# Kernel tuning notes

Hardware: AMD Instinct MI355X
Metric: run time of the kernel (lower is better)

## Reference

```python
import jax, jax.numpy as jnp
import numpy as np

N = 50000

def gcn_conv(x, W, b, src, dst, n_nodes):
    # PyG GCNConv: h = x @ W; add self-loops; sym-normalize; scatter-add; + bias
    h = x @ W  # [N, d_out]
    loop = jnp.arange(n_nodes, dtype=src.dtype)
    s = jnp.concatenate([src, loop])
    d = jnp.concatenate([dst, loop])
    deg = jax.ops.segment_sum(jnp.ones_like(d, dtype=h.dtype), d, num_segments=n_nodes)
    dinv = jnp.where(deg > 0, jax.lax.rsqrt(deg), 0.0)
    norm = dinv[s] * dinv[d]  # [E+N]
    msgs = h[s] * norm[:, None]  # gather + scale
    out = jax.ops.segment_sum(msgs, d, num_segments=n_nodes)  # scatter-add
    return out + b

def setup_inputs() -> dict:
    key = jax.random.key(0)
    k1, k2, k3, k4 = jax.random.split(key, 4)
    in_c, hid_c, out_c, E = 512, 256, 64, 800000
    x = jax.random.normal(k1, (N, in_c), dtype=jnp.float32)
    edge_index = jax.random.randint(k2, (2, E), 0, N, dtype=jnp.int64)
    W1 = jax.random.normal(k3, (in_c, hid_c), dtype=jnp.float32) / np.sqrt(in_c)
    b1 = jnp.zeros((hid_c,), dtype=jnp.float32)
    W2 = jax.random.normal(k4, (hid_c, out_c), dtype=jnp.float32) / np.sqrt(hid_c)
    b2 = jnp.zeros((out_c,), dtype=jnp.float32)
    return {"x": x, "edge_index": edge_index, "W1": W1, "b1": b1, "W2": W2, "b2": b2}

def reference(x, edge_index, W1, b1, W2, b2):
    src, dst = edge_index[0], edge_index[1]
    h = gcn_conv(x, W1, b1, src, dst, N)
    h = jax.nn.relu(h)
    h = gcn_conv(h, W2, b2, src, dst, N)
    return jax.nn.log_softmax(h, axis=1)
```

## Files before the change

kernel.cpp:

```cpp
#include <hip/hip_runtime.h>
#include <hip/hip_bf16.h>

#define IN_C 512
#define HID_C 256
#define OUT_C 64

typedef __attribute__((ext_vector_type(8))) short bf16x8;
typedef __attribute__((ext_vector_type(4))) float f32x4;

__device__ __forceinline__ ushort f2bf(float f) {
  __hip_bfloat16 h = __float2bfloat16(f);
  union { __hip_bfloat16 h; ushort u; } v; v.h = h; return v.u;
}
__device__ __forceinline__ void acc2(float& lo, float& hi, uint u) {
  union { uint i; float f; } a, b;
  a.i = u << 16; b.i = u & 0xffff0000u;
  lo += a.f; hi += b.f;
}


__global__ void deg_count(const int* __restrict__ dst, int* __restrict__ counts, int E) {
  int e = blockIdx.x * 256 + threadIdx.x;
  if (e >= E) return;
  atomicAdd(&counts[dst[e]], 1);
}

#define SCAN_TILE 1024

__global__ __launch_bounds__(256) void scan_block_sums(const int* __restrict__ counts,
                                                       int* __restrict__ partial, int n) {
  int base = blockIdx.x * SCAN_TILE + threadIdx.x * 4;
  int s = 0;
  if (base + 3 < n) {
    int4 v = *(const int4*)(counts + base);
    s = v.x + v.y + v.z + v.w;
  } else {
#pragma unroll
    for (int i = 0; i < 4; ++i) if (base + i < n) s += counts[base + i];
  }
#pragma unroll
  for (int off = 1; off < 64; off <<= 1) s += __shfl_xor(s, off);
  __shared__ int ws[4];
  int lane = threadIdx.x & 63, wid = threadIdx.x >> 6;
  if (lane == 0) ws[wid] = s;
  __syncthreads();
  if (threadIdx.x == 0) partial[blockIdx.x] = ws[0] + ws[1] + ws[2] + ws[3];
}

__global__ void scan_partials(int* __restrict__ partial, int nb) {
  int lane = threadIdx.x;
  int carry = 0;
  for (int base = 0; base < nb; base += 64) {
    int i = base + lane;
    int v = (i < nb) ? partial[i] : 0;
    int incl = v;
#pragma unroll
    for (int off = 1; off < 64; off <<= 1) {
      int y = __shfl_up(incl, off);
      if (lane >= off) incl += y;
    }
    if (i < nb) partial[i] = carry + incl - v;
    carry += __shfl(incl, 63);
  }
}

__global__ __launch_bounds__(256) void scan_write(const int* __restrict__ counts,
                                                  const int* __restrict__ partial,
                                                  int* __restrict__ offs,
                                                  int* __restrict__ cur,
                                                  float* __restrict__ dinv,
                                                  int n, int E) {
  int tid = threadIdx.x;
  int base = blockIdx.x * SCAN_TILE + tid * 4;
  int4 c = make_int4(0, 0, 0, 0);
  if (base + 3 < n) {
    c = *(const int4*)(counts + base);
  } else {
    if (base + 0 < n) c.x = counts[base + 0];
    if (base + 1 < n) c.y = counts[base + 1];
    if (base + 2 < n) c.z = counts[base + 2];
  }
  int tsum = c.x + c.y + c.z + c.w;
  int lane = tid & 63, wid = tid >> 6;
  int incl = tsum;
#pragma unroll
  for (int off = 1; off < 64; off <<= 1) {
    int y = __shfl_up(incl, off);
    if (lane >= off) incl += y;
  }
  __shared__ int ws[4];
  if (lane == 63) ws[wid] = incl;
  __syncthreads();
  int wbase = 0;
#pragma unroll
  for (int w = 0; w < 4; ++w) if (w < wid) wbase += ws[w];
  int off0 = partial[blockIdx.x] + wbase + (incl - tsum);
  int4 ov;
  ov.x = off0;
  ov.y = off0 + c.x;
  ov.z = off0 + c.x + c.y;
  ov.w = off0 + c.x + c.y + c.z;
  float4 dv;
  dv.x = rsqrtf((float)(c.x + 1));
  dv.y = rsqrtf((float)(c.y + 1));
  dv.z = rsqrtf((float)(c.z + 1));
  dv.w = rsqrtf((float)(c.w + 1));
  if (base + 3 < n) {
    *(int4*)(offs + base) = ov;
    *(int4*)(cur + base) = ov;
    *(float4*)(dinv + base) = dv;
  } else {
    int o4[4] = {ov.x, ov.y, ov.z, ov.w};
    float d4[4] = {dv.x, dv.y, dv.z, dv.w};
    for (int i = 0; i < 4; ++i)
      if (base + i < n) { offs[base + i] = o4[i]; cur[base + i] = o4[i]; dinv[base + i] = d4[i]; }
  }
  if (blockIdx.x == 0 && tid == 0) offs[n] = E;
}

__global__ void fill_adj(const int* __restrict__ src, const int* __restrict__ dst,
                         int* __restrict__ cur, int* __restrict__ adj, int E) {
  int e = blockIdx.x * 256 + threadIdx.x;
  if (e >= E) return;
  int pos = atomicAdd(&cur[dst[e]], 1);
  adj[pos] = src[e];
}

__global__ void convert_wt(const float* __restrict__ W, ushort* __restrict__ Wt, int K, int Ncol) {
  int idx = blockIdx.x * 256 + threadIdx.x;
  if (idx >= K * Ncol) return;
  int n = idx / K, k = idx % K;
  Wt[idx] = f2bf(W[(size_t)k * Ncol + n]);
}


#define LDP 56

__global__ __launch_bounds__(256) void gemm1(const float* __restrict__ A,
                                             const ushort* __restrict__ Bt,
                                             const float* __restrict__ dinv,
                                             ushort* __restrict__ C, int M) {
  __shared__ __align__(16) short As[128 * LDP];
  __shared__ __align__(16) short Bs[128 * LDP];
  int tid = threadIdx.x;
  int m0 = blockIdx.x * 128;
  int n0 = blockIdx.y * 128;
  int lane = tid & 63, wid = tid >> 6;
  int wm = (wid >> 1) * 64, wn = (wid & 1) * 64;
  f32x4 acc[4][4] = {};
  for (int k0 = 0; k0 < IN_C; k0 += 32) {
    {
      int tr = tid >> 3;
      int tc = (tid & 7) * 4;
#pragma unroll
      for (int i = 0; i < 4; ++i) {
        int row = tr + i * 32;
        int gm = m0 + row;
        float4 v = make_float4(0.f, 0.f, 0.f, 0.f);
        if (gm < M) v = *(const float4*)(A + (size_t)gm * IN_C + k0 + tc);
        uint2 p;
        p.x = (uint)f2bf(v.x) | ((uint)f2bf(v.y) << 16);
        p.y = (uint)f2bf(v.z) | ((uint)f2bf(v.w) << 16);
        *(uint2*)&As[row * LDP + tc] = p;
      }
    }
    {
#pragma unroll
      for (int i = 0; i < 2; ++i) {
        int chunk = tid + i * 256;
        int row = chunk >> 2;
        int c8 = (chunk & 3) * 8;
        uint4 v = *(const uint4*)(Bt + (size_t)(n0 + row) * IN_C + k0 + c8);
        *(uint4*)&Bs[row * LDP + c8] = v;
      }
    }
    __syncthreads();
    bf16x8 a[4], b[4];
    int kf = (lane >> 4) * 8;
    int rl = lane & 15;
#pragma unroll
    for (int i = 0; i < 4; ++i)
      a[i] = *(const bf16x8*)&As[(wm + i * 16 + rl) * LDP + kf];
#pragma unroll
    for (int j = 0; j < 4; ++j)
      b[j] = *(const bf16x8*)&Bs[(wn + j * 16 + rl) * LDP + kf];
#pragma unroll
    for (int i = 0; i < 4; ++i)
#pragma unroll
      for (int j = 0; j < 4; ++j)
        acc[i][j] = __builtin_amdgcn_mfma_f32_16x16x32_bf16(a[i], b[j], acc[i][j], 0, 0, 0);
    __syncthreads();
  }
  int r4 = (lane >> 4) * 4;
  int cl = lane & 15;
#pragma unroll
  for (int i = 0; i < 4; ++i) {
#pragma unroll
    for (int r = 0; r < 4; ++r) {
      int gr = m0 + wm + i * 16 + r4 + r;
      if (gr < M) {
        float dv = dinv[gr];
#pragma unroll
        for (int j = 0; j < 4; ++j) {
          int gc = n0 + wn + j * 16 + cl;
          C[(size_t)gr * HID_C + gc] = f2bf(dv * acc[i][j][r]);
        }
      }
    }
  }
}

__global__ __launch_bounds__(256) void gemm2(const ushort* __restrict__ A,
                                             const ushort* __restrict__ Bt,
                                             const float* __restrict__ dinv,
                                             ushort* __restrict__ C, int M) {
  __shared__ __align__(16) short As[128 * LDP];
  __shared__ __align__(16) short Bs[64 * LDP];
  int tid = threadIdx.x;
  int m0 = blockIdx.x * 128;
  int lane = tid & 63, wid = tid >> 6;
  int wm = wid * 32;
  f32x4 acc[2][4] = {};
  for (int k0 = 0; k0 < HID_C; k0 += 32) {
    {
#pragma unroll
      for (int i = 0; i < 2; ++i) {
        int chunk = tid + i * 256;
        int row = chunk >> 2;
        int c8 = (chunk & 3) * 8;
        int gm = m0 + row;
        uint4 v = make_uint4(0u, 0u, 0u, 0u);
        if (gm < M) v = *(const uint4*)(A + (size_t)gm * HID_C + k0 + c8);
        *(uint4*)&As[row * LDP + c8] = v;
      }
    }
    {
      int chunk = tid;
      int row = chunk >> 2;
      int c8 = (chunk & 3) * 8;
      uint4 v = *(const uint4*)(Bt + (size_t)row * HID_C + k0 + c8);
      *(uint4*)&Bs[row * LDP + c8] = v;
    }
    __syncthreads();
    bf16x8 a[2], b[4];
    int kf = (lane >> 4) * 8;
    int rl = lane & 15;
#pragma unroll
    for (int i = 0; i < 2; ++i)
      a[i] = *(const bf16x8*)&As[(wm + i * 16 + rl) * LDP + kf];
#pragma unroll
    for (int j = 0; j < 4; ++j)
      b[j] = *(const bf16x8*)&Bs[(j * 16 + rl) * LDP + kf];
#pragma unroll
    for (int i = 0; i < 2; ++i)
#pragma unroll
      for (int j = 0; j < 4; ++j)
        acc[i][j] = __builtin_amdgcn_mfma_f32_16x16x32_bf16(a[i], b[j], acc[i][j], 0, 0, 0);
    __syncthreads();
  }
  int r4 = (lane >> 4) * 4;
  int cl = lane & 15;
#pragma unroll
  for (int i = 0; i < 2; ++i) {
#pragma unroll
    for (int r = 0; r < 4; ++r) {
      int gr = m0 + wm + i * 16 + r4 + r;
      if (gr < M) {
        float dv = dinv[gr];
#pragma unroll
        for (int j = 0; j < 4; ++j) {
          int gc = j * 16 + cl;
          C[(size_t)gr * OUT_C + gc] = f2bf(dv * acc[i][j][r]);
        }
      }
    }
  }
}


__global__ __launch_bounds__(256) void agg1(const ushort* __restrict__ h,
                                            ushort* __restrict__ out,
                                            const float* __restrict__ dinv,
                                            const int* __restrict__ offs,
                                            const int* __restrict__ adj,
                                            const float* __restrict__ bias, int Nn) {
  int node = blockIdx.x * 4 + (threadIdx.x >> 6);
  if (node >= Nn) return;
  int lane = threadIdx.x & 63;
  int slot = lane >> 4;
  int c0 = (lane & 15) * 16;
  int e0 = offs[node];
  int cnt = offs[node + 1] - e0 + 1;
  float a[16];
#pragma unroll
  for (int i = 0; i < 16; ++i) a[i] = 0.f;
  for (int k = slot; k < cnt; k += 4) {
    int s = (k == 0) ? node : adj[e0 + k - 1];
    const uint4* rp = (const uint4*)(h + (size_t)s * HID_C + c0);
    uint4 u0 = rp[0];
    uint4 u1 = rp[1];
    acc2(a[0],  a[1],  u0.x);
    acc2(a[2],  a[3],  u0.y);
    acc2(a[4],  a[5],  u0.z);
    acc2(a[6],  a[7],  u0.w);
    acc2(a[8],  a[9],  u1.x);
    acc2(a[10], a[11], u1.y);
    acc2(a[12], a[13], u1.z);
    acc2(a[14], a[15], u1.w);
  }
#pragma unroll
  for (int i = 0; i < 16; ++i) {
    a[i] += __shfl_xor(a[i], 16);
    a[i] += __shfl_xor(a[i], 32);
  }
  if (lane < 16) {
    float dv = dinv[node];
    const float4* bp = (const float4*)(bias + c0);
    float bb[16];
#pragma unroll
    for (int q = 0; q < 4; ++q) {
      float4 b4 = bp[q];
      bb[q * 4 + 0] = b4.x; bb[q * 4 + 1] = b4.y;
      bb[q * 4 + 2] = b4.z; bb[q * 4 + 3] = b4.w;
    }
    uint r[8];
#pragma unroll
    for (int i = 0; i < 8; ++i) {
      float v0 = fmaxf(dv * a[2 * i]     + bb[2 * i],     0.f);
      float v1 = fmaxf(dv * a[2 * i + 1] + bb[2 * i + 1], 0.f);
      r[i] = (uint)f2bf(v0) | ((uint)f2bf(v1) << 16);
    }
    uint4* op = (uint4*)(out + (size_t)node * HID_C + c0);
    op[0] = make_uint4(r[0], r[1], r[2], r[3]);
    op[1] = make_uint4(r[4], r[5], r[6], r[7]);
  }
}

__global__ __launch_bounds__(256) void agg2(const ushort* __restrict__ h,
                                            float* __restrict__ out,
                                            const float* __restrict__ dinv,
                                            const int* __restrict__ offs,
                                            const int* __restrict__ adj,
                                            const float* __restrict__ bias, int Nn) {
  int node = blockIdx.x * 4 + (threadIdx.x >> 6);
  if (node >= Nn) return;
  int lane = threadIdx.x & 63;
  int slot = lane >> 3;
  int c0 = (lane & 7) * 8;
  int e0 = offs[node];
  int cnt = offs[node + 1] - e0 + 1;
  float a[8];
#pragma unroll
  for (int i = 0; i < 8; ++i) a[i] = 0.f;
  for (int k = slot; k < cnt; k += 8) {
    int s = (k == 0) ? node : adj[e0 + k - 1];
    uint4 u = *(const uint4*)(h + (size_t)s * OUT_C + c0);
    acc2(a[0], a[1], u.x);
    acc2(a[2], a[3], u.y);
    acc2(a[4], a[5], u.z);
    acc2(a[6], a[7], u.w);
  }
#pragma unroll
  for (int i = 0; i < 8; ++i) {
    a[i] += __shfl_xor(a[i], 8);
    a[i] += __shfl_xor(a[i], 16);
    a[i] += __shfl_xor(a[i], 32);
  }
  float dv = dinv[node];
  const float4* bp = (const float4*)(bias + c0);
  float4 bb0 = bp[0], bb1 = bp[1];
  float v[8];
  v[0] = dv * a[0] + bb0.x; v[1] = dv * a[1] + bb0.y;
  v[2] = dv * a[2] + bb0.z; v[3] = dv * a[3] + bb0.w;
  v[4] = dv * a[4] + bb1.x; v[5] = dv * a[5] + bb1.y;
  v[6] = dv * a[6] + bb1.z; v[7] = dv * a[7] + bb1.w;
  float m = v[0];
#pragma unroll
  for (int i = 1; i < 8; ++i) m = fmaxf(m, v[i]);
  m = fmaxf(m, __shfl_xor(m, 1));
  m = fmaxf(m, __shfl_xor(m, 2));
  m = fmaxf(m, __shfl_xor(m, 4));
  float s8 = 0.f;
#pragma unroll
  for (int i = 0; i < 8; ++i) s8 += expf(v[i] - m);
  s8 += __shfl_xor(s8, 1);
  s8 += __shfl_xor(s8, 2);
  s8 += __shfl_xor(s8, 4);
  float lg = logf(s8);
  if (lane < 8) {
    float4* op = (float4*)(out + (size_t)node * OUT_C + c0);
    op[0] = make_float4(v[0] - m - lg, v[1] - m - lg, v[2] - m - lg, v[3] - m - lg);
    op[1] = make_float4(v[4] - m - lg, v[5] - m - lg, v[6] - m - lg, v[7] - m - lg);
  }
}


extern "C" void kernel_launch(void* const* d_in, const int* in_sizes, int n_in,
                              void* d_out, int out_size, void* d_ws, size_t ws_size,
                              hipStream_t stream) {
  const float* x  = (const float*)d_in[0];
  const int*   ei = (const int*)d_in[1];
  const float* W1 = (const float*)d_in[2];
  const float* b1 = (const float*)d_in[3];
  const float* W2 = (const float*)d_in[4];
  const float* b2 = (const float*)d_in[5];
  float* outp = (float*)d_out;

  int Nn = in_sizes[0] / IN_C;
  int E  = in_sizes[1] / 2;
  const int* srcv = ei;
  const int* dstv = ei + E;

  char* ws = (char*)d_ws;
  size_t o = 0;
  auto alloc = [&](size_t bytes) {
    char* p = ws + o;
    o = (o + bytes + 255) & ~(size_t)255;
    return p;
  };
  float*  dinv  = (float*)alloc((size_t)Nn * 4);
  int*    counts= (int*)alloc((size_t)Nn * 4);
  int*    offs  = (int*)alloc((size_t)(Nn + 1) * 4);
  int*    cur   = (int*)alloc((size_t)Nn * 4);
  int*    adj   = (int*)alloc((size_t)E * 4);
  int*    partial=(int*)alloc((size_t)((Nn + SCAN_TILE - 1) / SCAN_TILE) * 4);
  ushort* W1t   = (ushort*)alloc((size_t)IN_C * HID_C * 2);
  ushort* W2t   = (ushort*)alloc((size_t)HID_C * OUT_C * 2);
  ushort* h1p   = (ushort*)alloc((size_t)Nn * HID_C * 2);
  ushort* h1a   = (ushort*)alloc((size_t)Nn * HID_C * 2);
  ushort* h2p   = (ushort*)alloc((size_t)Nn * OUT_C * 2);

  int eb = (E + 255) / 256;
  int sb = (Nn + SCAN_TILE - 1) / SCAN_TILE;

  hipMemsetAsync(counts, 0, (size_t)Nn * 4, stream);
  deg_count<<<eb, 256, 0, stream>>>(dstv, counts, E);
  scan_block_sums<<<sb, 256, 0, stream>>>(counts, partial, Nn);
  scan_partials<<<1, 64, 0, stream>>>(partial, sb);
  scan_write<<<sb, 256, 0, stream>>>(counts, partial, offs, cur, dinv, Nn, E);
  fill_adj<<<eb, 256, 0, stream>>>(srcv, dstv, cur, adj, E);
  convert_wt<<<(IN_C * HID_C + 255) / 256, 256, 0, stream>>>(W1, W1t, IN_C, HID_C);
  convert_wt<<<(HID_C * OUT_C + 255) / 256, 256, 0, stream>>>(W2, W2t, HID_C, OUT_C);

  gemm1<<<dim3((Nn + 127) / 128, HID_C / 128), 256, 0, stream>>>(x, W1t, dinv, h1p, Nn);
  agg1<<<(Nn + 3) / 4, 256, 0, stream>>>(h1p, h1a, dinv, offs, adj, b1, Nn);
  gemm2<<<(Nn + 127) / 128, 256, 0, stream>>>(h1a, W2t, dinv, h2p, Nn);
  agg2<<<(Nn + 3) / 4, 256, 0, stream>>>(h2p, outp, dinv, offs, adj, b2, Nn);
}
```

Before: 279.0 us.

## Pre-convert x to bf16 and double-buffer GEMMs with direct global-to-LDS loads

Adds a pass that converts x to bf16 into workspace, then uses a new gemm1 that streams bf16 tiles straight into LDS via global_load_lds with double buffering, so the next k-tile loads while the current one computes. gemm2 is rewritten the same way. The aim is to hide global-load latency and remove register staging. The cost is an extra read/write pass over x (about 100MB of fp32 read plus a bf16 write), and the unpadded 32-wide LDS rows may cause bank conflicts. It falls back to the old fp32 path when the workspace is too small.

```diff
diff --git a/kernel.cpp b/kernel.cpp
--- a/kernel.cpp
+++ b/kernel.cpp
@@ -16,6 +16,11 @@
   union { uint i; float f; } a, b;
   a.i = u << 16; b.i = u & 0xffff0000u;
   lo += a.f; hi += b.f;
+}
+__device__ __forceinline__ void glds16(const ushort* g, ushort* l) {
+  __builtin_amdgcn_global_load_lds(
+      (const __attribute__((address_space(1))) unsigned int*)(const void*)g,
+      (__attribute__((address_space(3))) unsigned int*)(void*)l, 16, 0, 0);
 }
 
 
@@ -133,13 +138,102 @@
   Wt[idx] = f2bf(W[(size_t)k * Ncol + n]);
 }
 
+__global__ __launch_bounds__(256) void convert_x(const float* __restrict__ x,
+                                                 ushort* __restrict__ xb, long n8) {
+  long stride = (long)gridDim.x * 256;
+  for (long i = (long)blockIdx.x * 256 + threadIdx.x; i < n8; i += stride) {
+    const float4* p = (const float4*)(x + i * 8);
+    float4 v0 = p[0], v1 = p[1];
+    uint4 o;
+    o.x = (uint)f2bf(v0.x) | ((uint)f2bf(v0.y) << 16);
+    o.y = (uint)f2bf(v0.z) | ((uint)f2bf(v0.w) << 16);
+    o.z = (uint)f2bf(v1.x) | ((uint)f2bf(v1.y) << 16);
+    o.w = (uint)f2bf(v1.z) | ((uint)f2bf(v1.w) << 16);
+    *(uint4*)(xb + i * 8) = o;
+  }
+}
+
+
+__global__ __launch_bounds__(256) void gemm1_bf(const ushort* __restrict__ A,
+                                                const ushort* __restrict__ Bt,
+                                                const float* __restrict__ dinv,
+                                                ushort* __restrict__ C, int M) {
+  __shared__ __align__(16) ushort As[2][128 * 32];
+  __shared__ __align__(16) ushort Bs[2][128 * 32];
+  int tid = threadIdx.x;
+  int lane = tid & 63, wid = tid >> 6;
+  int m0 = blockIdx.x * 128;
+  int n0 = blockIdx.y * 128;
+  int ca = wid * 64 + lane;
+  int rowa0 = ca >> 2, cola0 = (ca & 3) * 8;
+  int rowa1 = (ca + 256) >> 2, cola1 = (ca & 3) * 8;
+  int gma0 = m0 + rowa0; if (gma0 >= M) gma0 = M - 1;
+  int gma1 = m0 + rowa1; if (gma1 >= M) gma1 = M - 1;
+  const ushort* gA0 = A + (size_t)gma0 * IN_C + cola0;
+  const ushort* gA1 = A + (size_t)gma1 * IN_C + cola1;
+  const ushort* gB0 = Bt + (size_t)(n0 + rowa0) * IN_C + cola0;
+  const ushort* gB1 = Bt + (size_t)(n0 + rowa1) * IN_C + cola1;
+
+  int wm = (wid >> 1) * 64, wn = (wid & 1) * 64;
+  int kf = (lane >> 4) * 8, rl = lane & 15;
+  f32x4 acc[4][4] = {};
+
+  glds16(gA0, &As[0][ca * 8]);
+  glds16(gA1, &As[0][ca * 8 + 2048]);
+  glds16(gB0, &Bs[0][ca * 8]);
+  glds16(gB1, &Bs[0][ca * 8 + 2048]);
+  __syncthreads();
+
+  int cur = 0;
+  for (int t = 0; t < 16; ++t) {
+    if (t < 15) {
+      int k0 = (t + 1) * 32;
+      int nxt = cur ^ 1;
+      glds16(gA0 + k0, &As[nxt][ca * 8]);
+      glds16(gA1 + k0, &As[nxt][ca * 8 + 2048]);
+      glds16(gB0 + k0, &Bs[nxt][ca * 8]);
+      glds16(gB1 + k0, &Bs[nxt][ca * 8 + 2048]);
+    }
+    bf16x8 a[4], b[4];
+#pragma unroll
+    for (int i = 0; i < 4; ++i)
+      a[i] = *(const bf16x8*)&As[cur][(wm + i * 16 + rl) * 32 + kf];
+#pragma unroll
+    for (int j = 0; j < 4; ++j)
+      b[j] = *(const bf16x8*)&Bs[cur][(wn + j * 16 + rl) * 32 + kf];
+#pragma unroll
+    for (int i = 0; i < 4; ++i)
+#pragma unroll
+      for (int j = 0; j < 4; ++j)
+        acc[i][j] = __builtin_amdgcn_mfma_f32_16x16x32_bf16(a[i], b[j], acc[i][j], 0, 0, 0);
+    __syncthreads();
+    cur ^= 1;
+  }
+
+  int r4 = (lane >> 4) * 4;
+  int cl = lane & 15;
+#pragma unroll
+  for (int i = 0; i < 4; ++i) {
+#pragma unroll
+    for (int r = 0; r < 4; ++r) {
+      int gr = m0 + wm + i * 16 + r4 + r;
+      if (gr < M) {
+        float dv = dinv[gr];
+#pragma unroll
+        for (int j = 0; j < 4; ++j) {
+          int gc = n0 + wn + j * 16 + cl;
+          C[(size_t)gr * HID_C + gc] = f2bf(dv * acc[i][j][r]);
+        }
+      }
+    }
+  }
+}
 
 #define LDP 56
-
-__global__ __launch_bounds__(256) void gemm1(const float* __restrict__ A,
-                                             const ushort* __restrict__ Bt,
-                                             const float* __restrict__ dinv,
-                                             ushort* __restrict__ C, int M) {
+__global__ __launch_bounds__(256) void gemm1_f32(const float* __restrict__ A,
+                                                 const ushort* __restrict__ Bt,
+                                                 const float* __restrict__ dinv,
+                                                 ushort* __restrict__ C, int M) {
   __shared__ __align__(16) short As[128 * LDP];
   __shared__ __align__(16) short Bs[128 * LDP];
   int tid = threadIdx.x;
@@ -214,50 +308,54 @@
                                              const ushort* __restrict__ Bt,
                                              const float* __restrict__ dinv,
                                              ushort* __restrict__ C, int M) {
-  __shared__ __align__(16) short As[128 * LDP];
-  __shared__ __align__(16) short Bs[64 * LDP];
+  __shared__ __align__(16) ushort As[2][128 * 32];
+  __shared__ __align__(16) ushort Bs[2][64 * 32];
   int tid = threadIdx.x;
+  int lane = tid & 63, wid = tid >> 6;
   int m0 = blockIdx.x * 128;
-  int lane = tid & 63, wid = tid >> 6;
+  int ca = wid * 64 + lane;
+  int rowa0 = ca >> 2, cola0 = (ca & 3) * 8;
+  int rowa1 = (ca + 256) >> 2;
+  int gma0 = m0 + rowa0; if (gma0 >= M) gma0 = M - 1;
+  int gma1 = m0 + rowa1; if (gma1 >= M) gma1 = M - 1;
+  const ushort* gA0 = A + (size_t)gma0 * HID_C + cola0;
+  const ushort* gA1 = A + (size_t)gma1 * HID_C + cola0;
+  const ushort* gB0 = Bt + (size_t)rowa0 * HID_C + cola0;
+
   int wm = wid * 32;
+  int kf = (lane >> 4) * 8, rl = lane & 15;
   f32x4 acc[2][4] = {};
-  for (int k0 = 0; k0 < HID_C; k0 += 32) {
-    {
-#pragma unroll
-      for (int i = 0; i < 2; ++i) {
-        int chunk = tid + i * 256;
-        int row = chunk >> 2;
-        int c8 = (chunk & 3) * 8;
-        int gm = m0 + row;
-        uint4 v = make_uint4(0u, 0u, 0u, 0u);
-        if (gm < M) v = *(const uint4*)(A + (size_t)gm * HID_C + k0 + c8);
-        *(uint4*)&As[row * LDP + c8] = v;
-      }
-    }
-    {
-      int chunk = tid;
-      int row = chunk >> 2;
-      int c8 = (chunk & 3) * 8;
-      uint4 v = *(const uint4*)(Bt + (size_t)row * HID_C + k0 + c8);
-      *(uint4*)&Bs[row * LDP + c8] = v;
-    }
-    __syncthreads();
+
+  glds16(gA0, &As[0][ca * 8]);
+  glds16(gA1, &As[0][ca * 8 + 2048]);
+  glds16(gB0, &Bs[0][ca * 8]);
+  __syncthreads();
+
+  int cur = 0;
+  for (int t = 0; t < 8; ++t) {
+    if (t < 7) {
+      int k0 = (t + 1) * 32;
+      int nxt = cur ^ 1;
+      glds16(gA0 + k0, &As[nxt][ca * 8]);
+      glds16(gA1 + k0, &As[nxt][ca * 8 + 2048]);
+      glds16(gB0 + k0, &Bs[nxt][ca * 8]);
+    }
     bf16x8 a[2], b[4];
-    int kf = (lane >> 4) * 8;
-    int rl = lane & 15;
 #pragma unroll
     for (int i = 0; i < 2; ++i)
-      a[i] = *(const bf16x8*)&As[(wm + i * 16 + rl) * LDP + kf];
+      a[i] = *(const bf16x8*)&As[cur][(wm + i * 16 + rl) * 32 + kf];
 #pragma unroll
     for (int j = 0; j < 4; ++j)
-      b[j] = *(const bf16x8*)&Bs[(j * 16 + rl) * LDP + kf];
+      b[j] = *(const bf16x8*)&Bs[cur][(j * 16 + rl) * 32 + kf];
 #pragma unroll
     for (int i = 0; i < 2; ++i)
 #pragma unroll
       for (int j = 0; j < 4; ++j)
         acc[i][j] = __builtin_amdgcn_mfma_f32_16x16x32_bf16(a[i], b[j], acc[i][j], 0, 0, 0);
     __syncthreads();
-  }
+    cur ^= 1;
+  }
+
   int r4 = (lane >> 4) * 4;
   int cl = lane & 15;
 #pragma unroll
@@ -429,6 +527,9 @@
   ushort* h1p   = (ushort*)alloc((size_t)Nn * HID_C * 2);
   ushort* h1a   = (ushort*)alloc((size_t)Nn * HID_C * 2);
   ushort* h2p   = (ushort*)alloc((size_t)Nn * OUT_C * 2);
+  size_t xb_bytes = (size_t)Nn * IN_C * 2;
+  bool use_bf = (o + xb_bytes) <= ws_size;
+  ushort* xb = use_bf ? (ushort*)alloc(xb_bytes) : nullptr;
 
   int eb = (E + 255) / 256;
   int sb = (Nn + SCAN_TILE - 1) / SCAN_TILE;
@@ -442,7 +543,14 @@
   convert_wt<<<(IN_C * HID_C + 255) / 256, 256, 0, stream>>>(W1, W1t, IN_C, HID_C);
   convert_wt<<<(HID_C * OUT_C + 255) / 256, 256, 0, stream>>>(W2, W2t, HID_C, OUT_C);
 
-  gemm1<<<dim3((Nn + 127) / 128, HID_C / 128), 256, 0, stream>>>(x, W1t, dinv, h1p, Nn);
+  if (use_bf) {
+    long n8 = (long)Nn * IN_C / 8;
+    int cb = (int)((n8 + 255) / 256); if (cb > 2048) cb = 2048;
+    convert_x<<<cb, 256, 0, stream>>>(x, xb, n8);
+    gemm1_bf<<<dim3((Nn + 127) / 128, HID_C / 128), 256, 0, stream>>>(xb, W1t, dinv, h1p, Nn);
+  } else {
+    gemm1_f32<<<dim3((Nn + 127) / 128, HID_C / 128), 256, 0, stream>>>(x, W1t, dinv, h1p, Nn);
+  }
   agg1<<<(Nn + 3) / 4, 256, 0, stream>>>(h1p, h1a, dinv, offs, adj, b1, Nn);
   gemm2<<<(Nn + 127) / 128, 256, 0, stream>>>(h1a, W2t, dinv, h2p, Nn);
   agg2<<<(Nn + 3) / 4, 256, 0, stream>>>(h2p, outp, dinv, offs, adj, b2, Nn);
```

Result: faster. 257.1 us (-7.8%).
